# Performance work log

Measured on AMD Instinct MI355X. Metric: run time of the kernel, lower is better.

Reference implementation:

```python
import jax, jax.numpy as jnp
import numpy as np

ALPHA = 0.5

def setup_inputs() -> dict:
    key = jax.random.key(0)
    k1, k2 = jax.random.split(key)
    B, S, F_IN, F_OUT = 64, 512, 1024, 1024
    x = jax.random.normal(k1, (B, S, F_IN), dtype=jnp.float32)
    W = jax.random.normal(k2, (F_OUT, F_IN), dtype=jnp.float32) * (F_IN ** -0.5)
    return {"x": x, "W": W}

def reference(x, W):
    # x: [B, S, F_in], W: [F_out, F_in] (torch Linear layout, no bias)
    alpha = jnp.asarray(ALPHA, dtype=x.dtype)
    # Project all segments at once (the big GEMM), then scan the EMA recurrence.
    y = jnp.einsum('bsf,of->bso', x, W)  # [B, S, F_out]
    y_t = jnp.swapaxes(y, 0, 1)          # [S, B, F_out] for scan over segments

    def step(h, yk):
        h = alpha * h + (1 - alpha) * yk
        return h, h

    h0 = jnp.zeros((x.shape[0], W.shape[0]), dtype=x.dtype)
    hk, hiddens_t = jax.lax.scan(step, h0, y_t)
    hiddens = jnp.swapaxes(hiddens_t, 0, 1)  # [B, S, F_out]
    return (hk, hiddens)
```

## Files before the change

### kernel.cpp

```cpp
#include <hip/hip_runtime.h>
#include <hip/hip_bf16.h>
#include <stdint.h>

#define B_DIM 64
#define S_DIM 512
#define K_DIM 1024
#define N_DIM 1024
#define M_DIM (B_DIM * S_DIM)
#define N_TILES 256

typedef __attribute__((ext_vector_type(8))) short short8;
typedef __attribute__((ext_vector_type(4))) float floatx4;

__device__ __forceinline__ uint4 pack8_bf16(float4 a, float4 b) {
  union { unsigned short u[8]; uint4 q; } pk;
  __hip_bfloat16 t;
  t = __float2bfloat16(a.x); pk.u[0] = *(unsigned short*)&t;
  t = __float2bfloat16(a.y); pk.u[1] = *(unsigned short*)&t;
  t = __float2bfloat16(a.z); pk.u[2] = *(unsigned short*)&t;
  t = __float2bfloat16(a.w); pk.u[3] = *(unsigned short*)&t;
  t = __float2bfloat16(b.x); pk.u[4] = *(unsigned short*)&t;
  t = __float2bfloat16(b.y); pk.u[5] = *(unsigned short*)&t;
  t = __float2bfloat16(b.z); pk.u[6] = *(unsigned short*)&t;
  t = __float2bfloat16(b.w); pk.u[7] = *(unsigned short*)&t;
  return pk.q;
}

__global__ __launch_bounds__(256) void prep_kernel(
    const float* __restrict__ W, __hip_bfloat16* __restrict__ Wb,
    const float* __restrict__ x, __hip_bfloat16* __restrict__ wx) {
  if (blockIdx.x < 512) {
    const size_t t = (size_t)blockIdx.x * 256 + threadIdx.x;
    float4 v0 = *(const float4*)(W + t * 8);
    float4 v1 = *(const float4*)(W + t * 8 + 4);
    *(uint4*)(Wb + t * 8) = pack8_bf16(v0, v1);
  } else {
    const int t = blockIdx.x - 512;
    const int b = t >> 2;
    const int c = t & 3;
    const int k4 = threadIdx.x * 4;
    float4 acc = {0.f, 0.f, 0.f, 0.f};
    if (c != 0) {
      const float* base = x + ((size_t)b * S_DIM + c * 128) * K_DIM + k4;
      float wgt = 0.5f;
      #pragma unroll
      for (int j = 1; j <= 16; ++j) {
        float4 v = *(const float4*)(base - (size_t)j * K_DIM);
        acc.x += wgt * v.x; acc.y += wgt * v.y;
        acc.z += wgt * v.z; acc.w += wgt * v.w;
        wgt *= 0.5f;
      }
    }
    union { unsigned short u[4]; uint2 q; } pk;
    __hip_bfloat16 h;
    h = __float2bfloat16(acc.x); pk.u[0] = *(unsigned short*)&h;
    h = __float2bfloat16(acc.y); pk.u[1] = *(unsigned short*)&h;
    h = __float2bfloat16(acc.z); pk.u[2] = *(unsigned short*)&h;
    h = __float2bfloat16(acc.w); pk.u[3] = *(unsigned short*)&h;
    *(uint2*)(wx + (size_t)t * K_DIM + k4) = pk.q;
  }
}

template <bool MAIN>
__global__ __launch_bounds__(256) void gemm_tmpl(
    const void* __restrict__ Aptr,
    const __hip_bfloat16* __restrict__ Bw,
    float* __restrict__ out,
    const float* __restrict__ warm) {
  __shared__ __hip_bfloat16 lA[128 * 64];
  __shared__ __hip_bfloat16 lB[128 * 64];
  __shared__ float hbuf[128];

  const int tid  = threadIdx.x;
  const int lane = tid & 63;
  const int w    = tid >> 6;
  const int wm   = (w >> 1) * 64;
  const int wn   = (w & 1) * 64;
  const int quad = lane >> 4;
  const int l15  = lane & 15;
  const int r7   = l15 & 7;

  int m0, n0;
  if (MAIN) {
    const int bi    = blockIdx.x;
    const int xcd   = bi & 7;
    const int local = bi >> 3;
    m0 = (xcd * 32 + (local >> 3)) * 128;
    n0 = (local & 7) * 128;
  } else {
    m0 = (blockIdx.x >> 3) * 128;
    n0 = (blockIdx.x & 7) * 128;
  }

  floatx4 acc[4][4] = {};

  for (int k0 = 0; k0 < K_DIM; k0 += 64) {
    #pragma unroll
    for (int p = 0; p < 4; ++p) {
      int c    = tid + p * 256;
      int r    = c >> 3;
      int slot = c & 7;
      int kc   = (slot ^ (r & 7)) * 8;
      const __hip_bfloat16* gb = Bw + (size_t)(n0 + r) * K_DIM + k0 + kc;
      __builtin_amdgcn_global_load_lds(
          (const __attribute__((address_space(1))) void*)gb,
          (__attribute__((address_space(3))) void*)&lB[c * 8], 16, 0, 0);
    }
    if constexpr (MAIN) {
      const float* Af = (const float*)Aptr;
      #pragma unroll
      for (int p = 0; p < 4; ++p) {
        int c = tid + p * 256;
        int r = c >> 3;
        int q = c & 7;
        const float* ga = Af + (size_t)(m0 + r) * K_DIM + k0 + q * 8;
        float4 v0 = *(const float4*)ga;
        float4 v1 = *(const float4*)(ga + 4);
        *(uint4*)&lA[r * 64 + ((q ^ (r & 7)) * 8)] = pack8_bf16(v0, v1);
      }
    } else {
      const __hip_bfloat16* Ab = (const __hip_bfloat16*)Aptr;
      #pragma unroll
      for (int p = 0; p < 4; ++p) {
        int c    = tid + p * 256;
        int r    = c >> 3;
        int slot = c & 7;
        int kc   = (slot ^ (r & 7)) * 8;
        const __hip_bfloat16* ga = Ab + (size_t)(m0 + r) * K_DIM + k0 + kc;
        __builtin_amdgcn_global_load_lds(
            (const __attribute__((address_space(1))) void*)ga,
            (__attribute__((address_space(3))) void*)&lA[c * 8], 16, 0, 0);
      }
    }
    __syncthreads();

    #pragma unroll
    for (int kk = 0; kk < 64; kk += 32) {
      const int q0 = kk >> 3;
      short8 af[4], bfr[4];
      #pragma unroll
      for (int i = 0; i < 4; ++i) {
        af[i]  = *(const short8*)&lA[(wm + i * 16 + l15) * 64 +
                                     (((q0 + quad) ^ r7) * 8)];
        bfr[i] = *(const short8*)&lB[(wn + i * 16 + l15) * 64 +
                                     (((q0 + quad) ^ r7) * 8)];
      }
      #pragma unroll
      for (int i = 0; i < 4; ++i)
        #pragma unroll
        for (int j = 0; j < 4; ++j)
          acc[i][j] = __builtin_amdgcn_mfma_f32_16x16x32_bf16(
              af[i], bfr[j], acc[i][j], 0, 0, 0);
    }
    __syncthreads();
  }

  if (MAIN) {
    const float fq = (quad == 0) ? 1.f : (quad == 1) ? 0.0625f
                   : (quad == 2) ? 0.00390625f : 2.44140625e-4f;
    const int tile = m0 >> 7;
    #pragma unroll
    for (int j = 0; j < 4; ++j) {
      const int colIdx = wn + j * 16 + l15;
      float Wst = 0.f;
      if (w < 2) Wst = warm[(size_t)tile * N_DIM + n0 + colIdx];
      #pragma unroll
      for (int i = 0; i < 4; ++i) {
        const float y0 = acc[i][j][0], y1 = acc[i][j][1];
        const float y2 = acc[i][j][2], y3 = acc[i][j][3];
        const float L0 = 0.5f * y0;
        const float L1 = 0.5f * (L0 + y1);
        const float L2 = 0.5f * (L1 + y2);
        const float L3 = 0.5f * (L2 + y3);
        float P = L3;
        float t1 = __shfl_up(P, 16);
        if (quad >= 1) P += 0.0625f * t1;
        float t2 = __shfl_up(P, 32);
        if (quad >= 2) P += 0.00390625f * t2;
        float H = __shfl_up(P, 16);
        H = (quad >= 1) ? H : 0.f;
        const float S = H + fq * Wst;
        acc[i][j][0] = L0 + 0.5f    * S;
        acc[i][j][1] = L1 + 0.25f   * S;
        acc[i][j][2] = L2 + 0.125f  * S;
        acc[i][j][3] = L3 + 0.0625f * S;
        const float F = __shfl(P, 48 + l15);
        Wst = F + 1.52587890625e-05f * Wst;
      }
      if (w < 2 && quad == 0) hbuf[colIdx] = Wst;
    }
    __syncthreads();
    if (w >= 2) {
      #pragma unroll
      for (int j = 0; j < 4; ++j) {
        const float Z = hbuf[wn + j * 16 + l15] * fq;
        #pragma unroll
        for (int i = 0; i < 4; ++i) {
          const float fi = (i == 0) ? 1.f
                         : (i == 1) ? 1.52587890625e-05f
                         : (i == 2) ? 2.3283064365386963e-10f
                                    : 3.552713678800501e-15f;
          const float base = fi * Z;
          acc[i][j][0] += 0.5f    * base;
          acc[i][j][1] += 0.25f   * base;
          acc[i][j][2] += 0.125f  * base;
          acc[i][j][3] += 0.0625f * base;
        }
      }
    }
  }

  float* hid = MAIN ? out + B_DIM * N_DIM : out;
  #pragma unroll
  for (int i = 0; i < 4; ++i) {
    #pragma unroll
    for (int j = 0; j < 4; ++j) {
      #pragma unroll
      for (int r = 0; r < 4; ++r) {
        int gm = m0 + wm + i * 16 + quad * 4 + r;
        int gn = n0 + wn + j * 16 + l15;
        float v = acc[i][j][r];
        hid[(size_t)gm * N_DIM + gn] = v;
        if (MAIN && ((gm & (S_DIM - 1)) == (S_DIM - 1))) {
          out[(size_t)(gm >> 9) * N_DIM + gn] = v;
        }
      }
    }
  }
}

extern "C" void kernel_launch(void* const* d_in, const int* in_sizes, int n_in,
                              void* d_out, int out_size, void* d_ws, size_t ws_size,
                              hipStream_t stream) {
  const float* x = (const float*)d_in[0];
  const float* W = (const float*)d_in[1];
  float* out = (float*)d_out;

  __hip_bfloat16* Wb = (__hip_bfloat16*)d_ws;
  __hip_bfloat16* wx = Wb + (size_t)N_DIM * K_DIM;
  float*          wy = (float*)(wx + (size_t)N_TILES * K_DIM);

  prep_kernel<<<dim3(768), dim3(256), 0, stream>>>(W, Wb, x, wx);
  gemm_tmpl<false><<<dim3(16), dim3(256), 0, stream>>>(wx, Wb, wy, nullptr);
  gemm_tmpl<true><<<dim3((M_DIM / 128) * (N_DIM / 128)), dim3(256), 0, stream>>>(x, Wb, out, wy);
}
```

Before: 366.1 us.

## Double-buffer LDS tiles and prefetch next fp32 A tile into registers

After: 400.7 us. 1.09x slower.

```diff
diff --git a/kernel.cpp b/kernel.cpp
--- a/kernel.cpp
+++ b/kernel.cpp
@@ -28,7 +28,7 @@
 
 __global__ __launch_bounds__(256) void prep_kernel(
     const float* __restrict__ W, __hip_bfloat16* __restrict__ Wb,
-    const float* __restrict__ x, __hip_bfloat16* __restrict__ wx) {
+    const float* __restrict__ x, float* __restrict__ wx) {
   if (blockIdx.x < 512) {
     const size_t t = (size_t)blockIdx.x * 256 + threadIdx.x;
     float4 v0 = *(const float4*)(W + t * 8);
@@ -51,24 +51,18 @@
         wgt *= 0.5f;
       }
     }
-    union { unsigned short u[4]; uint2 q; } pk;
-    __hip_bfloat16 h;
-    h = __float2bfloat16(acc.x); pk.u[0] = *(unsigned short*)&h;
-    h = __float2bfloat16(acc.y); pk.u[1] = *(unsigned short*)&h;
-    h = __float2bfloat16(acc.z); pk.u[2] = *(unsigned short*)&h;
-    h = __float2bfloat16(acc.w); pk.u[3] = *(unsigned short*)&h;
-    *(uint2*)(wx + (size_t)t * K_DIM + k4) = pk.q;
+    *(float4*)(wx + (size_t)t * K_DIM + k4) = acc;
   }
 }
 
 template <bool MAIN>
 __global__ __launch_bounds__(256) void gemm_tmpl(
-    const void* __restrict__ Aptr,
+    const float* __restrict__ Af,
     const __hip_bfloat16* __restrict__ Bw,
     float* __restrict__ out,
     const float* __restrict__ warm) {
-  __shared__ __hip_bfloat16 lA[128 * 64];
-  __shared__ __hip_bfloat16 lB[128 * 64];
+  __shared__ __hip_bfloat16 lA[2][128 * 64];
+  __shared__ __hip_bfloat16 lB[2][128 * 64];
   __shared__ float hbuf[128];
 
   const int tid  = threadIdx.x;
@@ -92,47 +86,55 @@
     n0 = (blockIdx.x & 7) * 128;
   }
 
+  float4 areg[4][2];
+
   floatx4 acc[4][4] = {};
 
-  for (int k0 = 0; k0 < K_DIM; k0 += 64) {
-    #pragma unroll
-    for (int p = 0; p < 4; ++p) {
-      int c    = tid + p * 256;
-      int r    = c >> 3;
-      int slot = c & 7;
-      int kc   = (slot ^ (r & 7)) * 8;
-      const __hip_bfloat16* gb = Bw + (size_t)(n0 + r) * K_DIM + k0 + kc;
-      __builtin_amdgcn_global_load_lds(
-          (const __attribute__((address_space(1))) void*)gb,
-          (__attribute__((address_space(3))) void*)&lB[c * 8], 16, 0, 0);
-    }
-    if constexpr (MAIN) {
-      const float* Af = (const float*)Aptr;
+  #pragma unroll
+  for (int p = 0; p < 4; ++p) {
+    int c = tid + p * 256, r = c >> 3, q = c & 7;
+    const float* ga = Af + (size_t)(m0 + r) * K_DIM + q * 8;
+    areg[p][0] = *(const float4*)ga;
+    areg[p][1] = *(const float4*)(ga + 4);
+  }
+  #pragma unroll
+  for (int p = 0; p < 4; ++p) {
+    int c = tid + p * 256, r = c >> 3, slot = c & 7;
+    int kc = (slot ^ (r & 7)) * 8;
+    const __hip_bfloat16* gb = Bw + (size_t)(n0 + r) * K_DIM + kc;
+    __builtin_amdgcn_global_load_lds(
+        (const __attribute__((address_space(1))) void*)gb,
+        (__attribute__((address_space(3))) void*)&lB[0][c * 8], 16, 0, 0);
+  }
+  #pragma unroll
+  for (int p = 0; p < 4; ++p) {
+    int c = tid + p * 256, r = c >> 3, q = c & 7;
+    *(uint4*)&lA[0][r * 64 + ((q ^ (r & 7)) * 8)] =
+        pack8_bf16(areg[p][0], areg[p][1]);
+  }
+  __syncthreads();
+
+  int cur = 0;
+  for (int t = 0; t < 16; ++t) {
+    const int k1 = (t + 1) * 64;
+    if (t < 15) {
       #pragma unroll
       for (int p = 0; p < 4; ++p) {
-        int c = tid + p * 256;
-        int r = c >> 3;
-        int q = c & 7;
-        const float* ga = Af + (size_t)(m0 + r) * K_DIM + k0 + q * 8;
-        float4 v0 = *(const float4*)ga;
-        float4 v1 = *(const float4*)(ga + 4);
-        *(uint4*)&lA[r * 64 + ((q ^ (r & 7)) * 8)] = pack8_bf16(v0, v1);
-      }
-    } else {
-      const __hip_bfloat16* Ab = (const __hip_bfloat16*)Aptr;
+        int c = tid + p * 256, r = c >> 3, q = c & 7;
+        const float* ga = Af + (size_t)(m0 + r) * K_DIM + k1 + q * 8;
+        areg[p][0] = *(const float4*)ga;
+        areg[p][1] = *(const float4*)(ga + 4);
+      }
       #pragma unroll
       for (int p = 0; p < 4; ++p) {
-        int c    = tid + p * 256;
-        int r    = c >> 3;
-        int slot = c & 7;
-        int kc   = (slot ^ (r & 7)) * 8;
-        const __hip_bfloat16* ga = Ab + (size_t)(m0 + r) * K_DIM + k0 + kc;
+        int c = tid + p * 256, r = c >> 3, slot = c & 7;
+        int kc = (slot ^ (r & 7)) * 8;
+        const __hip_bfloat16* gb = Bw + (size_t)(n0 + r) * K_DIM + k1 + kc;
         __builtin_amdgcn_global_load_lds(
-            (const __attribute__((address_space(1))) void*)ga,
-            (__attribute__((address_space(3))) void*)&lA[c * 8], 16, 0, 0);
-      }
-    }
-    __syncthreads();
+            (const __attribute__((address_space(1))) void*)gb,
+            (__attribute__((address_space(3))) void*)&lB[cur ^ 1][c * 8], 16, 0, 0);
+      }
+    }
 
     #pragma unroll
     for (int kk = 0; kk < 64; kk += 32) {
@@ -140,10 +142,10 @@
       short8 af[4], bfr[4];
       #pragma unroll
       for (int i = 0; i < 4; ++i) {
-        af[i]  = *(const short8*)&lA[(wm + i * 16 + l15) * 64 +
-                                     (((q0 + quad) ^ r7) * 8)];
-        bfr[i] = *(const short8*)&lB[(wn + i * 16 + l15) * 64 +
-                                     (((q0 + quad) ^ r7) * 8)];
+        af[i]  = *(const short8*)&lA[cur][(wm + i * 16 + l15) * 64 +
+                                          (((q0 + quad) ^ r7) * 8)];
+        bfr[i] = *(const short8*)&lB[cur][(wn + i * 16 + l15) * 64 +
+                                          (((q0 + quad) ^ r7) * 8)];
       }
       #pragma unroll
       for (int i = 0; i < 4; ++i)
@@ -152,7 +154,17 @@
           acc[i][j] = __builtin_amdgcn_mfma_f32_16x16x32_bf16(
               af[i], bfr[j], acc[i][j], 0, 0, 0);
     }
+
+    if (t < 15) {
+      #pragma unroll
+      for (int p = 0; p < 4; ++p) {
+        int c = tid + p * 256, r = c >> 3, q = c & 7;
+        *(uint4*)&lA[cur ^ 1][r * 64 + ((q ^ (r & 7)) * 8)] =
+            pack8_bf16(areg[p][0], areg[p][1]);
+      }
+    }
     __syncthreads();
+    cur ^= 1;
   }
 
   if (MAIN) {
@@ -237,8 +249,8 @@
   float* out = (float*)d_out;
 
   __hip_bfloat16* Wb = (__hip_bfloat16*)d_ws;
-  __hip_bfloat16* wx = Wb + (size_t)N_DIM * K_DIM;
-  float*          wy = (float*)(wx + (size_t)N_TILES * K_DIM);
+  float*          wx = (float*)(Wb + (size_t)N_DIM * K_DIM);
+  float*          wy = wx + (size_t)N_TILES * K_DIM;
 
   prep_kernel<<<dim3(768), dim3(256), 0, stream>>>(W, Wb, x, wx);
   gemm_tmpl<false><<<dim3(16), dim3(256), 0, stream>>>(wx, Wb, wy, nullptr);
```
